# Performance work log

Hardware: AMD Instinct MI355X
Metric: run time of the kernel (lower is better)

Reference implementation:

```python
import jax, jax.numpy as jnp
import numpy as np

B, N, L = 1, 2048, 256
H, E = 24, 128
D = H * E          # query_dim = inner_dim = 3072
P = 1536           # added_kv_proj_dim
EPS = 1e-5


def _rope_tables(n, e):
    pos = np.arange(n, dtype=np.float32)
    inv_freq = 1.0 / (10000.0 ** (np.arange(0, e, 2, dtype=np.float32) / e))
    ang = pos[:, None] * inv_freq[None, :]          # [n, e/2]
    ang = np.repeat(ang, 2, axis=-1)                # interleaved pairs -> [n, e]
    return np.cos(ang).astype(np.float32), np.sin(ang).astype(np.float32)


def _trans_mat(e):
    # rotate-pairs matrix: (x @ tm)[2i] = -x[2i+1], (x @ tm)[2i+1] = x[2i]
    tm = np.zeros((e, e), dtype=np.float32)
    idx = np.arange(0, e, 2)
    tm[idx + 1, idx] = -1.0
    tm[idx, idx + 1] = 1.0
    return tm


def setup_inputs() -> dict:
    key = jax.random.key(0)
    ks = jax.random.split(key, 16)
    s = 0.02
    cos, sin = _rope_tables(N, E)
    return {
        "spatial": jax.random.normal(ks[0], (B, N, D), jnp.float32),
        "prompt": jax.random.normal(ks[1], (B, L, P), jnp.float32),
        "w_qkv": jax.random.normal(ks[2], (D, 3 * D), jnp.float32) * s,
        "w_add_qkv": jax.random.normal(ks[3], (P, 3 * D), jnp.float32) * s,
        "b_add_qkv": jax.random.normal(ks[4], (3 * D,), jnp.float32) * s,
        "norm_q_w": jnp.ones((E,), jnp.float32),
        "norm_k_w": jnp.ones((E,), jnp.float32),
        "norm_add_q_w": jnp.ones((E,), jnp.float32),
        "norm_add_k_w": jnp.ones((E,), jnp.float32),
        "w_out": jax.random.normal(ks[5], (D, D), jnp.float32) * s,
        "b_out": jax.random.normal(ks[6], (D,), jnp.float32) * s,
        "w_add_out": jax.random.normal(ks[7], (D, D), jnp.float32) * s,
        "b_add_out": jax.random.normal(ks[8], (D,), jnp.float32) * s,
        "rope_cos": jnp.asarray(cos),
        "rope_sin": jnp.asarray(sin),
        "trans_mat": jnp.asarray(_trans_mat(E)),
        "N": N,
    }


def _rms(x, w):
    return x * jax.lax.rsqrt(jnp.mean(x * x, axis=-1, keepdims=True) + EPS) * w


def _split_heads(x, h, e):
    b, s, _ = x.shape
    return x.reshape(b, s, h, e).transpose(0, 2, 1, 3)  # [B,H,S,E]


def reference(spatial, prompt, w_qkv, w_add_qkv, b_add_qkv,
              norm_q_w, norm_k_w, norm_add_q_w, norm_add_k_w,
              w_out, b_out, w_add_out, b_add_out,
              rope_cos, rope_sin, trans_mat, N):
    e = norm_q_w.shape[0]
    h = w_qkv.shape[1] // (3 * e)
    b, n, _ = spatial.shape

    # fused QKV for spatial stream (no bias)
    q, k, v = jnp.split(spatial @ w_qkv, 3, axis=-1)
    q, k, v = (_split_heads(t, h, e) for t in (q, k, v))   # [B,H,N,E]
    q = _rms(q, norm_q_w)
    k = _rms(k, norm_k_w)

    # fused QKV for prompt stream (with bias)
    aq, ak, av = jnp.split(prompt @ w_add_qkv + b_add_qkv, 3, axis=-1)
    aq, ak, av = (_split_heads(t, h, e) for t in (aq, ak, av))  # [B,H,L,E]
    aq = _rms(aq, norm_add_q_w)
    ak = _rms(ak, norm_add_k_w)

    # RoPE on spatial q/k: x*cos + (x@trans_mat)*sin
    def rope(x):
        return x * rope_cos + jnp.einsum('bhne,ef->bhnf', x, trans_mat) * rope_sin
    q = rope(q)
    k = rope(k)

    # joint attention, 'rear' strategy: prompt KV appended after spatial KV
    qf = jnp.concatenate([q, aq], axis=2)   # [B,H,N+L,E]
    kf = jnp.concatenate([k, ak], axis=2)
    vf = jnp.concatenate([v, av], axis=2)
    scale = 1.0 / jnp.sqrt(jnp.float32(e))
    scores = jnp.einsum('bhqe,bhke->bhqk', qf, kf) * scale
    attn = jax.nn.softmax(scores, axis=-1)
    out = jnp.einsum('bhqk,bhke->bhqe', attn, vf)           # [B,H,N+L,E]

    def merge(x):
        return x.transpose(0, 2, 1, 3).reshape(b, x.shape[2], h * e)

    spatial_out = merge(out[:, :, :n]) @ w_out + b_out      # [B,N,D]
    prompt_out = merge(out[:, :, n:]) @ w_add_out + b_add_out  # [B,L,D]
    return spatial_out, prompt_out
```

## Files before the change

### kernel.cpp

```cpp
#include <hip/hip_runtime.h>
#include <cstdint>
#include <cstddef>

typedef __attribute__((ext_vector_type(8))) short short8;
typedef __attribute__((ext_vector_type(4))) float f32x4;
typedef __attribute__((ext_vector_type(16))) float f32x16;

#define DEVI static __device__ __forceinline__

DEVI float bf2f(unsigned short b) {
  union { unsigned int u; float f; } v; v.u = ((unsigned int)b) << 16; return v.f;
}
DEVI unsigned short f2bf(float f) {
  union { float f; unsigned int u; } v; v.f = f;
  unsigned int r = v.u + 0x7fffu + ((v.u >> 16) & 1u);
  return (unsigned short)(r >> 16);
}
DEVI unsigned int pk2(float a, float b) {
  union { float f; unsigned int u; } ua, ub; ua.f = a; ub.f = b;
  return ((ua.u + 0x8000u) >> 16) | ((ub.u + 0x8000u) & 0xffff0000u);
}

DEVI void gload16(const void* g, void* l) {
  __builtin_amdgcn_global_load_lds(
      (const __attribute__((address_space(1))) void*)g,
      (__attribute__((address_space(3))) void*)l, 16, 0, 0);
}

DEVI void drain_ldsdma() {
  asm volatile("s_waitcnt vmcnt(0)" ::: "memory");
  __builtin_amdgcn_sched_barrier(0);
}

__global__ __launch_bounds__(256) void f32_to_bf16_2(
    const float* __restrict__ a, unsigned short* __restrict__ oa, int n4a,
    const float* __restrict__ b, unsigned short* __restrict__ ob, int n4b)
{
  int i = blockIdx.x * blockDim.x + threadIdx.x;
  int stride = gridDim.x * blockDim.x;
  int total = n4a + n4b;
  for (; i < total; i += stride) {
    const float4* src = (i < n4a) ? &((const float4*)a)[i] : &((const float4*)b)[i - n4a];
    ushort4* dst = (i < n4a) ? &((ushort4*)oa)[i] : &((ushort4*)ob)[i - n4a];
    float4 f = *src;
    ushort4 u;
    u.x = f2bf(f.x); u.y = f2bf(f.y); u.z = f2bf(f.z); u.w = f2bf(f.w);
    *dst = u;
  }
}

DEVI void tr_body(const float* in, unsigned short* out, int Kd, int Nd,
                  int n0, int k0, unsigned short (*tile)[72], int t)
{
  int r = t >> 2, cg = (t & 3) * 16;
  const float* src = in + (size_t)(k0 + r) * Nd + n0 + cg;
#pragma unroll
  for (int q = 0; q < 16; q += 4) {
    float4 f = *(const float4*)(src + q);
    ushort4 u;
    u.x = f2bf(f.x); u.y = f2bf(f.y); u.z = f2bf(f.z); u.w = f2bf(f.w);
    *(ushort4*)&tile[r][cg + q] = u;
  }
  __syncthreads();
  unsigned int p[8];
#pragma unroll
  for (int q = 0; q < 8; ++q)
    p[q] = (unsigned int)tile[cg + 2*q][r] | ((unsigned int)tile[cg + 2*q + 1][r] << 16);
  unsigned short* dst = out + (size_t)(n0 + r) * Kd + k0 + cg;
  *(uint4*)dst       = make_uint4(p[0], p[1], p[2], p[3]);
  *(uint4*)(dst + 8) = make_uint4(p[4], p[5], p[6], p[7]);
}

__global__ __launch_bounds__(256) void transpose_wqkv(
    const float* __restrict__ w_qkv, const float* __restrict__ w_add_qkv,
    unsigned short* __restrict__ wTq, unsigned short* __restrict__ wTaq)
{
  __shared__ unsigned short tile[64][72];
  int y = blockIdx.y;
  const float* in;  unsigned short* out;  int Kd, k0;
  if (y < 48) { in = w_qkv;     out = wTq;  Kd = 3072; k0 = y * 64; }
  else        { in = w_add_qkv; out = wTaq; Kd = 1536; k0 = (y - 48) * 64; }
  tr_body(in, out, Kd, 9216, blockIdx.x * 64, k0, tile, threadIdx.x);
}

__global__ __launch_bounds__(256) void transpose_wout(
    const float* __restrict__ w_out, const float* __restrict__ w_add_out,
    unsigned short* __restrict__ wTo, unsigned short* __restrict__ wTao)
{
  __shared__ unsigned short tile[64][72];
  const float* in = blockIdx.z ? w_add_out : w_out;
  unsigned short* out = blockIdx.z ? wTao : wTo;
  tr_body(in, out, 3072, 3072, blockIdx.x * 64, blockIdx.y * 64, tile, threadIdx.x);
}

__global__ __launch_bounds__(256) void transpose_bf16_64(
    const unsigned short* __restrict__ in, unsigned short* __restrict__ out,
    int rows, int cols)
{
  __shared__ unsigned short tile[64][72];
  size_t hoff = (size_t)blockIdx.z * rows * cols;
  int e0 = blockIdx.x * 64, s0 = blockIdx.y * 64;
  int t = threadIdx.x;
  int r = t >> 2, cg = (t & 3) * 16;
  const unsigned short* src = in + hoff + (size_t)(s0 + r) * cols + e0 + cg;
  *(uint4*)&tile[r][cg]     = *(const uint4*)src;
  *(uint4*)&tile[r][cg + 8] = *(const uint4*)(src + 8);
  __syncthreads();
  unsigned int p[8];
#pragma unroll
  for (int q = 0; q < 8; ++q)
    p[q] = (unsigned int)tile[cg + 2*q][r] | ((unsigned int)tile[cg + 2*q + 1][r] << 16);
  unsigned short* dst = out + hoff + (size_t)(e0 + r) * rows + s0 + cg;
  *(uint4*)dst       = make_uint4(p[0], p[1], p[2], p[3]);
  *(uint4*)(dst + 8) = make_uint4(p[4], p[5], p[6], p[7]);
}

__global__ __launch_bounds__(256, 4) void gemm_qkv2(
    const unsigned short* __restrict__ Aspat, const unsigned short* __restrict__ Aprom,
    const unsigned short* __restrict__ Btq, const unsigned short* __restrict__ Btaq,
    const float* __restrict__ biasp, unsigned short* __restrict__ Cout)
{
  __shared__ unsigned short lsA[128 * 64];
  __shared__ unsigned short lsB[128 * 64];
  const int tid = threadIdx.x;
  const int w = tid >> 6, lane = tid & 63;
  const int wr = w >> 1, wc = w & 1;
  const int l15 = lane & 15, lhi = lane >> 4;
  const int wg = blockIdx.x;
  const int swz = (wg & 7) * 162 + (wg >> 3);
  const int bx = swz / 18, by = swz - bx * 18;
  const bool pr = by >= 16;
  const int K = pr ? 1536 : 3072;

  f32x4 acc[4][4];
#pragma unroll
  for (int i = 0; i < 4; ++i)
#pragma unroll
    for (int j = 0; j < 4; ++j) acc[i][j] = (f32x4){0.f, 0.f, 0.f, 0.f};

  int srcoff[4];
#pragma unroll
  for (int j = 0; j < 4; ++j) {
    int c = j * 256 + tid;
    int row = c >> 3;
    int sl = (c & 7) ^ (row & 7);
    srcoff[j] = row * K + sl * 8;
  }
  const int wb = w * 1024;
  const unsigned short* Abase = pr ? (Aprom + (size_t)((by - 16) * 128) * 1536)
                                   : (Aspat + (size_t)(by * 128) * 3072);
  const unsigned short* Bbase = (pr ? Btaq : Btq) + (size_t)(bx * 128) * K;

  for (int k0 = 0; k0 < K; k0 += 64) {
#pragma unroll
    for (int j = 0; j < 4; ++j) {
      gload16(Abase + srcoff[j] + k0, (char*)lsA + j * 4096 + wb);
      gload16(Bbase + srcoff[j] + k0, (char*)lsB + j * 4096 + wb);
    }
    __syncthreads();
#pragma unroll
    for (int kk = 0; kk < 2; ++kk) {
      const int sl = ((kk << 2) + lhi) ^ (l15 & 7);
      short8 af[4], bf[4];
#pragma unroll
      for (int t = 0; t < 4; ++t) {
        af[t] = *(const short8*)((char*)lsA + (wr * 64 + t * 16 + l15) * 128 + (sl << 4));
        bf[t] = *(const short8*)((char*)lsB + (wc * 64 + t * 16 + l15) * 128 + (sl << 4));
      }
#pragma unroll
      for (int mt = 0; mt < 4; ++mt)
#pragma unroll
        for (int nt = 0; nt < 4; ++nt)
          acc[mt][nt] = __builtin_amdgcn_mfma_f32_16x16x32_bf16(af[mt], bf[nt], acc[mt][nt], 0, 0, 0);
    }
    __syncthreads();
  }

  const int nbase = bx * 128 + wc * 64;
  const int mbase = by * 128 + wr * 64;
  float bv[4] = {0.f, 0.f, 0.f, 0.f};
  if (pr) {
#pragma unroll
    for (int nt = 0; nt < 4; ++nt) bv[nt] = biasp[nbase + nt * 16 + l15];
  }
#pragma unroll
  for (int mt = 0; mt < 4; ++mt)
#pragma unroll
    for (int nt = 0; nt < 4; ++nt) {
#pragma unroll
      for (int r2 = 0; r2 < 4; ++r2) {
        int m = mbase + mt * 16 + lhi * 4 + r2;
        int n = nbase + nt * 16 + l15;
        Cout[(size_t)m * 9216 + n] = f2bf(acc[mt][nt][r2] + bv[nt]);
      }
    }
}

__global__ __launch_bounds__(256, 4) void gemm_out2(
    const unsigned short* __restrict__ A,
    const unsigned short* __restrict__ Bt0, const float* __restrict__ b0,
    const unsigned short* __restrict__ Bt1, const float* __restrict__ b1,
    float* __restrict__ C)
{
  __shared__ unsigned short lsA[128 * 64];
  __shared__ unsigned short lsB[128 * 64];
  const int tid = threadIdx.x;
  const int w = tid >> 6, lane = tid & 63;
  const int wr = w >> 1, wc = w & 1;
  const int l15 = lane & 15, lhi = lane >> 4;
  const int wg = blockIdx.x;
  const int swz = (wg & 7) * 54 + (wg >> 3);
  const int bx = swz / 18, by = swz - bx * 18;
  const bool pr = by >= 16;

  f32x4 acc[4][4];
#pragma unroll
  for (int i = 0; i < 4; ++i)
#pragma unroll
    for (int j = 0; j < 4; ++j) acc[i][j] = (f32x4){0.f, 0.f, 0.f, 0.f};

  int srcoff[4];
#pragma unroll
  for (int j = 0; j < 4; ++j) {
    int c = j * 256 + tid;
    int row = c >> 3;
    int sl = (c & 7) ^ (row & 7);
    srcoff[j] = row * 3072 + sl * 8;
  }
  const int wb = w * 1024;
  const unsigned short* Abase = A + (size_t)(by * 128) * 3072;
  const unsigned short* Bbase = (pr ? Bt1 : Bt0) + (size_t)(bx * 128) * 3072;
  const float* bias = pr ? b1 : b0;

  for (int k0 = 0; k0 < 3072; k0 += 64) {
#pragma unroll
    for (int j = 0; j < 4; ++j) {
      gload16(Abase + srcoff[j] + k0, (char*)lsA + j * 4096 + wb);
      gload16(Bbase + srcoff[j] + k0, (char*)lsB + j * 4096 + wb);
    }
    __syncthreads();
#pragma unroll
    for (int kk = 0; kk < 2; ++kk) {
      const int sl = ((kk << 2) + lhi) ^ (l15 & 7);
      short8 af[4], bf[4];
#pragma unroll
      for (int t = 0; t < 4; ++t) {
        af[t] = *(const short8*)((char*)lsA + (wr * 64 + t * 16 + l15) * 128 + (sl << 4));
        bf[t] = *(const short8*)((char*)lsB + (wc * 64 + t * 16 + l15) * 128 + (sl << 4));
      }
#pragma unroll
      for (int mt = 0; mt < 4; ++mt)
#pragma unroll
        for (int nt = 0; nt < 4; ++nt)
          acc[mt][nt] = __builtin_amdgcn_mfma_f32_16x16x32_bf16(af[mt], bf[nt], acc[mt][nt], 0, 0, 0);
    }
    __syncthreads();
  }

  const int nbase = bx * 128 + wc * 64;
  const int mbase = by * 128 + wr * 64;
  float bv[4];
#pragma unroll
  for (int nt = 0; nt < 4; ++nt) bv[nt] = bias[nbase + nt * 16 + l15];
#pragma unroll
  for (int mt = 0; mt < 4; ++mt)
#pragma unroll
    for (int nt = 0; nt < 4; ++nt) {
#pragma unroll
      for (int r2 = 0; r2 < 4; ++r2) {
        int m = mbase + mt * 16 + lhi * 4 + r2;
        int n = nbase + nt * 16 + l15;
        C[(size_t)m * 3072 + n] = acc[mt][nt][r2] + bv[nt];
      }
    }
}

__global__ __launch_bounds__(256) void fuse_rms_rope(
    const unsigned short* __restrict__ qkv,
    const unsigned short* __restrict__ aqkv,
    const float* __restrict__ nq, const float* __restrict__ nk,
    const float* __restrict__ naq, const float* __restrict__ nak,
    const float* __restrict__ ctab, const float* __restrict__ stab,
    unsigned short* __restrict__ Qf, unsigned short* __restrict__ Kf,
    unsigned short* __restrict__ Vf)
{
  int wid = blockIdx.x * 4 + (threadIdx.x >> 6);
  int lane = threadIdx.x & 63;
  int h = wid / 2304, s = wid % 2304;
  bool sp = (s < 2048);
  const unsigned short* src = sp ? (qkv + (size_t)s * 9216)
                                 : (aqkv + (size_t)(s - 2048) * 9216);
  int e = lane * 2;
  ushort2 qu = *(const ushort2*)&src[h * 128 + e];
  ushort2 ku = *(const ushort2*)&src[3072 + h * 128 + e];
  ushort2 vu = *(const ushort2*)&src[6144 + h * 128 + e];
  float q0 = bf2f(qu.x), q1 = bf2f(qu.y);
  float k0 = bf2f(ku.x), k1 = bf2f(ku.y);
  float sq = q0 * q0 + q1 * q1, sk = k0 * k0 + k1 * k1;
#pragma unroll
  for (int mm = 1; mm < 64; mm <<= 1) {
    sq += __shfl_xor(sq, mm);
    sk += __shfl_xor(sk, mm);
  }
  float rq = rsqrtf(sq * (1.f / 128.f) + 1e-5f);
  float rk = rsqrtf(sk * (1.f / 128.f) + 1e-5f);
  const float* wq = sp ? nq : naq;
  const float* wk = sp ? nk : nak;
  q0 *= rq * wq[e]; q1 *= rq * wq[e + 1];
  k0 *= rk * wk[e]; k1 *= rk * wk[e + 1];
  if (sp) {
    float c0 = ctab[s * 128 + e], c1 = ctab[s * 128 + e + 1];
    float s0 = stab[s * 128 + e], s1 = stab[s * 128 + e + 1];
    float a0 = q0 * c0 - q1 * s0, a1 = q1 * c1 + q0 * s1;
    float b0 = k0 * c0 - k1 * s0, b1 = k1 * c1 + k0 * s1;
    q0 = a0; q1 = a1; k0 = b0; k1 = b1;
  }
  const float scale = 0.08838834764831845f * 1.4426950408889634f;
  q0 *= scale; q1 *= scale;
  size_t o = (size_t)h * 2304 * 128 + (size_t)s * 128 + e;
  *(ushort2*)&Qf[o] = make_ushort2(f2bf(q0), f2bf(q1));
  *(ushort2*)&Kf[o] = make_ushort2(f2bf(k0), f2bf(k1));
  *(ushort2*)&Vf[o] = vu;
}

__global__ __launch_bounds__(256, 2) void attn_fwd(
    const unsigned short* __restrict__ Qf, const unsigned short* __restrict__ Kf,
    const unsigned short* __restrict__ Vt, unsigned short* __restrict__ Om)
{
  __shared__ unsigned short lsK[2][64 * 128];
  __shared__ unsigned short lsV[2][128 * 64];
  int wg = blockIdx.x;
  int swz = (wg & 7) * 54 + (wg >> 3);
  int h = swz / 18, qt = swz - h * 18;
  int q0 = qt * 128;
  int tid = threadIdx.x, w = tid >> 6, lane = tid & 63;
  int l31 = lane & 31, hh = lane >> 5;
  const size_t headO = (size_t)h * 2304 * 128;

  short8 qf[8];
  {
    const unsigned short* qrow = Qf + headO + (size_t)(q0 + w * 32 + l31) * 128 + hh * 8;
#pragma unroll
    for (int s = 0; s < 8; ++s)
      qf[s] = *(const short8*)(qrow + s * 16);
  }

  float m_run = -1e30f, lsum = 0.f;
  f32x16 accO[4];
#pragma unroll
  for (int dt = 0; dt < 4; ++dt)
#pragma unroll
    for (int i = 0; i < 16; ++i) accO[dt][i] = 0.f;

  size_t kGo[4], vGo[4];
  int loff[4];
#pragma unroll
  for (int j = 0; j < 4; ++j) {
    int c = j * 256 + w * 64 + lane;
    int krow = c >> 4, kcol = (c & 15) ^ (krow & 7);
    int vrow = c >> 3, vcol = (c & 7) ^ (vrow & 7);
    kGo[j] = (size_t)krow * 128 + kcol * 8;
    vGo[j] = (size_t)vrow * 2304 + vcol * 8;
    loff[j] = (j * 256 + w * 64) * 16;
  }
  const unsigned short* kbase0 = Kf + headO;
  const unsigned short* vbase0 = Vt + headO;

  auto stage = [&](int kb2, int b) {
    const unsigned short* kb_ = kbase0 + (size_t)kb2 * 128;
    const unsigned short* vb_ = vbase0 + kb2;
#pragma unroll
    for (int j = 0; j < 4; ++j) {
      gload16(kb_ + kGo[j], (char*)lsK[b] + loff[j]);
      gload16(vb_ + vGo[j], (char*)lsV[b] + loff[j]);
    }
  };

  stage(0, 0);
  int cur = 0;

  for (int kb = 0; kb < 2304; kb += 64) {
    drain_ldsdma();
    __syncthreads();
    if (kb + 64 < 2304) stage(kb + 64, cur ^ 1);

    f32x16 accS[2];
#pragma unroll
    for (int t = 0; t < 2; ++t)
#pragma unroll
      for (int i = 0; i < 16; ++i) accS[t][i] = 0.f;
    __builtin_amdgcn_s_setprio(1);
#pragma unroll
    for (int t = 0; t < 2; ++t) {
      const int row = l31 + t * 32;
      const int rsw = row & 7;
#pragma unroll
      for (int s = 0; s < 8; ++s) {
        short8 kfr = *(const short8*)((char*)lsK[cur] + row * 256 +
                        (((s * 2 + hh) ^ rsw) << 4));
        accS[t] = __builtin_amdgcn_mfma_f32_32x32x16_bf16(kfr, qf[s], accS[t], 0, 0, 0);
      }
    }
    __builtin_amdgcn_s_setprio(0);

    float lm = accS[0][0];
#pragma unroll
    for (int t = 0; t < 2; ++t)
#pragma unroll
      for (int i = 0; i < 16; ++i) lm = fmaxf(lm, accS[t][i]);
    float lmx = fmaxf(lm, __shfl_xor(lm, 32));
    if (!__all(lmx <= m_run + 11.0f)) {
      float mnew = fmaxf(m_run, lmx);
      float corr = __builtin_amdgcn_exp2f(m_run - mnew);
      lsum *= corr;
      float corrq[16];
#pragma unroll
      for (int r = 0; r < 16; ++r)
        corrq[r] = __shfl(corr, ((r & 3) + 8 * (r >> 2) + 4 * hh) | (lane & 32));
#pragma unroll
      for (int dt = 0; dt < 4; ++dt)
#pragma unroll
        for (int r = 0; r < 16; ++r) accO[dt][r] *= corrq[r];
      m_run = mnew;
    }
#pragma unroll
    for (int t = 0; t < 2; ++t)
#pragma unroll
      for (int i = 0; i < 16; ++i) {
        float p = __builtin_amdgcn_exp2f(accS[t][i] - m_run);
        accS[t][i] = p;
        lsum += p;
      }

    __builtin_amdgcn_s_setprio(1);
#pragma unroll
    for (int ks = 0; ks < 4; ++ks) {
      const int t = ks >> 1;
      const int qlo = 8 * (ks & 1);
      unsigned int wlo0 = pk2(accS[t][qlo + 0], accS[t][qlo + 1]);
      unsigned int wlo1 = pk2(accS[t][qlo + 2], accS[t][qlo + 3]);
      unsigned int whi0 = pk2(accS[t][qlo + 4], accS[t][qlo + 5]);
      unsigned int whi1 = pk2(accS[t][qlo + 6], accS[t][qlo + 7]);
      unsigned int r0 = __shfl_xor(hh ? wlo0 : whi0, 32);
      unsigned int r1 = __shfl_xor(hh ? wlo1 : whi1, 32);
      unsigned int fw0 = hh ? r0 : wlo0;
      unsigned int fw1 = hh ? r1 : wlo1;
      unsigned int fw2 = hh ? whi0 : r0;
      unsigned int fw3 = hh ? whi1 : r1;
      unsigned int fwa[4] = {fw0, fw1, fw2, fw3};
      short8 paf = *(short8*)fwa;
#pragma unroll
      for (int dt = 0; dt < 4; ++dt) {
        const int row = dt * 32 + l31;
        short8 vfr = *(const short8*)((char*)lsV[cur] + row * 128 +
                        (((ks * 2 + hh) ^ (row & 7)) << 4));
        accO[dt] = __builtin_amdgcn_mfma_f32_32x32x16_bf16(paf, vfr, accO[dt], 0, 0, 0);
      }
    }
    __builtin_amdgcn_s_setprio(0);
    cur ^= 1;
  }

  lsum += __shfl_xor(lsum, 32);
  float inv = 1.0f / lsum;
  float invq[16];
#pragma unroll
  for (int r = 0; r < 16; ++r)
    invq[r] = __shfl(inv, ((r & 3) + 8 * (r >> 2) + 4 * hh) | (lane & 32));
#pragma unroll
  for (int dt = 0; dt < 4; ++dt)
#pragma unroll
    for (int r = 0; r < 16; ++r) {
      int qrow = (r & 3) + 8 * (r >> 2) + 4 * hh;
      int row = q0 + w * 32 + qrow;
      Om[(size_t)row * 3072 + h * 128 + dt * 32 + l31] = f2bf(accO[dt][r] * invq[r]);
    }
}

extern "C" void kernel_launch(void* const* d_in, const int* in_sizes, int n_in,
                              void* d_out, int out_size, void* d_ws, size_t ws_size,
                              hipStream_t stream)
{
  const float* spatial      = (const float*)d_in[0];
  const float* prompt       = (const float*)d_in[1];
  const float* w_qkv        = (const float*)d_in[2];
  const float* w_add_qkv    = (const float*)d_in[3];
  const float* b_add_qkv    = (const float*)d_in[4];
  const float* norm_q_w     = (const float*)d_in[5];
  const float* norm_k_w     = (const float*)d_in[6];
  const float* norm_add_q_w = (const float*)d_in[7];
  const float* norm_add_k_w = (const float*)d_in[8];
  const float* w_out        = (const float*)d_in[9];
  const float* b_out        = (const float*)d_in[10];
  const float* w_add_out    = (const float*)d_in[11];
  const float* b_add_out    = (const float*)d_in[12];
  const float* rope_cos     = (const float*)d_in[13];
  const float* rope_sin     = (const float*)d_in[14];

  constexpr size_t O_WTQ  = 0;
  constexpr size_t O_WTAQ = 56623104;
  constexpr size_t O_SPAT = 84934656;
  constexpr size_t O_PROM = 97517568;
  constexpr size_t O_QKV  = 98304000;
  constexpr size_t O_AQKV = 136052736;
  constexpr size_t O_QF   = 140771328;
  constexpr size_t O_KF   = 154927104;
  constexpr size_t O_VF   = 169082880;
  constexpr size_t TOTAL  = 183238656;
  constexpr size_t O_WTO  = O_WTQ;
  constexpr size_t O_WTAO = O_WTQ + 18874368;
  constexpr size_t O_VT   = O_QKV;
  constexpr size_t O_ATTN = O_WTAQ;
  if (ws_size < TOTAL) return;

  char* ws = (char*)d_ws;
  unsigned short* wTq      = (unsigned short*)(ws + O_WTQ);
  unsigned short* wTaq     = (unsigned short*)(ws + O_WTAQ);
  unsigned short* spat_bf  = (unsigned short*)(ws + O_SPAT);
  unsigned short* prom_bf  = (unsigned short*)(ws + O_PROM);
  unsigned short* qkv_s    = (unsigned short*)(ws + O_QKV);
  unsigned short* aqkv     = (unsigned short*)(ws + O_AQKV);
  unsigned short* Qf       = (unsigned short*)(ws + O_QF);
  unsigned short* Kf       = (unsigned short*)(ws + O_KF);
  unsigned short* Vf       = (unsigned short*)(ws + O_VF);
  unsigned short* wTo      = (unsigned short*)(ws + O_WTO);
  unsigned short* wTao     = (unsigned short*)(ws + O_WTAO);
  unsigned short* Vt       = (unsigned short*)(ws + O_VT);
  unsigned short* attn_out = (unsigned short*)(ws + O_ATTN);

  f32_to_bf16_2<<<2048, 256, 0, stream>>>(spatial, spat_bf, 2048 * 3072 / 4,
                                          prompt, prom_bf, 256 * 1536 / 4);
  transpose_wqkv<<<dim3(144, 72), 256, 0, stream>>>(w_qkv, w_add_qkv, wTq, wTaq);
  gemm_qkv2<<<1296, 256, 0, stream>>>(spat_bf, prom_bf, wTq, wTaq, b_add_qkv, qkv_s);
  fuse_rms_rope<<<13824, 256, 0, stream>>>(qkv_s, aqkv, norm_q_w, norm_k_w,
                                           norm_add_q_w, norm_add_k_w,
                                           rope_cos, rope_sin, Qf, Kf, Vf);
  transpose_bf16_64<<<dim3(2, 36, 24), 256, 0, stream>>>(Vf, Vt, 2304, 128);
  attn_fwd<<<432, 256, 0, stream>>>(Qf, Kf, Vt, attn_out);
  transpose_wout<<<dim3(48, 48, 2), 256, 0, stream>>>(w_out, w_add_out, wTo, wTao);
  gemm_out2<<<432, 256, 0, stream>>>(attn_out, wTo, b_out, wTao, b_add_out,
                                     (float*)d_out);
}
```

Measured before the change: 401.4 us.

## Double query rows per wave in attention to reuse K/V LDS fragments

Each wave now handles two 32-row query blocks (256 query rows per workgroup) and keeps two sets of online-softmax state and output accumulators. Every K and V fragment read from LDS feeds two MFMAs, which halves LDS reads and K/V global staging per query. The grid shrinks from 432 to 216 workgroups and launch bounds drop to one block per SIMD. This raises register pressure and cuts occupancy and parallelism on a device with 256 CUs.

```diff
diff --git a/kernel.cpp b/kernel.cpp
--- a/kernel.cpp
+++ b/kernel.cpp
@@ -323,34 +323,37 @@
   *(ushort2*)&Vf[o] = vu;
 }
 
-__global__ __launch_bounds__(256, 2) void attn_fwd(
+__global__ __launch_bounds__(256, 1) void attn_fwd(
     const unsigned short* __restrict__ Qf, const unsigned short* __restrict__ Kf,
     const unsigned short* __restrict__ Vt, unsigned short* __restrict__ Om)
 {
   __shared__ unsigned short lsK[2][64 * 128];
   __shared__ unsigned short lsV[2][128 * 64];
   int wg = blockIdx.x;
-  int swz = (wg & 7) * 54 + (wg >> 3);
-  int h = swz / 18, qt = swz - h * 18;
-  int q0 = qt * 128;
+  int swz = (wg & 7) * 27 + (wg >> 3);
+  int h = swz / 9, qt = swz - h * 9;
+  int q0 = qt * 256;
   int tid = threadIdx.x, w = tid >> 6, lane = tid & 63;
   int l31 = lane & 31, hh = lane >> 5;
   const size_t headO = (size_t)h * 2304 * 128;
 
-  short8 qf[8];
+  short8 qfa[8], qfb[8];
   {
-    const unsigned short* qrow = Qf + headO + (size_t)(q0 + w * 32 + l31) * 128 + hh * 8;
-#pragma unroll
-    for (int s = 0; s < 8; ++s)
-      qf[s] = *(const short8*)(qrow + s * 16);
-  }
-
-  float m_run = -1e30f, lsum = 0.f;
-  f32x16 accO[4];
+    const unsigned short* qra = Qf + headO + (size_t)(q0 + w * 64 + l31) * 128 + hh * 8;
+    const unsigned short* qrb = qra + 32 * 128;
+#pragma unroll
+    for (int s = 0; s < 8; ++s) {
+      qfa[s] = *(const short8*)(qra + s * 16);
+      qfb[s] = *(const short8*)(qrb + s * 16);
+    }
+  }
+
+  float m0 = -1e30f, m1 = -1e30f, ls0 = 0.f, ls1 = 0.f;
+  f32x16 accO0[4], accO1[4];
 #pragma unroll
   for (int dt = 0; dt < 4; ++dt)
 #pragma unroll
-    for (int i = 0; i < 16; ++i) accO[dt][i] = 0.f;
+    for (int i = 0; i < 16; ++i) { accO0[dt][i] = 0.f; accO1[dt][i] = 0.f; }
 
   size_t kGo[4], vGo[4];
   int loff[4];
@@ -384,96 +387,144 @@
     __syncthreads();
     if (kb + 64 < 2304) stage(kb + 64, cur ^ 1);
 
-    f32x16 accS[2];
-#pragma unroll
-    for (int t = 0; t < 2; ++t)
-#pragma unroll
-      for (int i = 0; i < 16; ++i) accS[t][i] = 0.f;
-    __builtin_amdgcn_s_setprio(1);
 #pragma unroll
     for (int t = 0; t < 2; ++t) {
-      const int row = l31 + t * 32;
-      const int rsw = row & 7;
-#pragma unroll
-      for (int s = 0; s < 8; ++s) {
-        short8 kfr = *(const short8*)((char*)lsK[cur] + row * 256 +
-                        (((s * 2 + hh) ^ rsw) << 4));
-        accS[t] = __builtin_amdgcn_mfma_f32_32x32x16_bf16(kfr, qf[s], accS[t], 0, 0, 0);
-      }
-    }
-    __builtin_amdgcn_s_setprio(0);
-
-    float lm = accS[0][0];
-#pragma unroll
-    for (int t = 0; t < 2; ++t)
-#pragma unroll
-      for (int i = 0; i < 16; ++i) lm = fmaxf(lm, accS[t][i]);
-    float lmx = fmaxf(lm, __shfl_xor(lm, 32));
-    if (!__all(lmx <= m_run + 11.0f)) {
-      float mnew = fmaxf(m_run, lmx);
-      float corr = __builtin_amdgcn_exp2f(m_run - mnew);
-      lsum *= corr;
-      float corrq[16];
-#pragma unroll
-      for (int r = 0; r < 16; ++r)
-        corrq[r] = __shfl(corr, ((r & 3) + 8 * (r >> 2) + 4 * hh) | (lane & 32));
-#pragma unroll
-      for (int dt = 0; dt < 4; ++dt)
-#pragma unroll
-        for (int r = 0; r < 16; ++r) accO[dt][r] *= corrq[r];
-      m_run = mnew;
-    }
-#pragma unroll
-    for (int t = 0; t < 2; ++t)
-#pragma unroll
-      for (int i = 0; i < 16; ++i) {
-        float p = __builtin_amdgcn_exp2f(accS[t][i] - m_run);
-        accS[t][i] = p;
-        lsum += p;
-      }
-
-    __builtin_amdgcn_s_setprio(1);
-#pragma unroll
-    for (int ks = 0; ks < 4; ++ks) {
-      const int t = ks >> 1;
-      const int qlo = 8 * (ks & 1);
-      unsigned int wlo0 = pk2(accS[t][qlo + 0], accS[t][qlo + 1]);
-      unsigned int wlo1 = pk2(accS[t][qlo + 2], accS[t][qlo + 3]);
-      unsigned int whi0 = pk2(accS[t][qlo + 4], accS[t][qlo + 5]);
-      unsigned int whi1 = pk2(accS[t][qlo + 6], accS[t][qlo + 7]);
-      unsigned int r0 = __shfl_xor(hh ? wlo0 : whi0, 32);
-      unsigned int r1 = __shfl_xor(hh ? wlo1 : whi1, 32);
-      unsigned int fw0 = hh ? r0 : wlo0;
-      unsigned int fw1 = hh ? r1 : wlo1;
-      unsigned int fw2 = hh ? whi0 : r0;
-      unsigned int fw3 = hh ? whi1 : r1;
-      unsigned int fwa[4] = {fw0, fw1, fw2, fw3};
-      short8 paf = *(short8*)fwa;
-#pragma unroll
-      for (int dt = 0; dt < 4; ++dt) {
-        const int row = dt * 32 + l31;
-        short8 vfr = *(const short8*)((char*)lsV[cur] + row * 128 +
-                        (((ks * 2 + hh) ^ (row & 7)) << 4));
-        accO[dt] = __builtin_amdgcn_mfma_f32_32x32x16_bf16(paf, vfr, accO[dt], 0, 0, 0);
-      }
-    }
-    __builtin_amdgcn_s_setprio(0);
+      f32x16 aS0, aS1;
+#pragma unroll
+      for (int i = 0; i < 16; ++i) { aS0[i] = 0.f; aS1[i] = 0.f; }
+
+      __builtin_amdgcn_s_setprio(1);
+      {
+        const int row = l31 + t * 32;
+        const int rsw = row & 7;
+#pragma unroll
+        for (int s = 0; s < 8; ++s) {
+          short8 kfr = *(const short8*)((char*)lsK[cur] + row * 256 +
+                          (((s * 2 + hh) ^ rsw) << 4));
+          aS0 = __builtin_amdgcn_mfma_f32_32x32x16_bf16(kfr, qfa[s], aS0, 0, 0, 0);
+          aS1 = __builtin_amdgcn_mfma_f32_32x32x16_bf16(kfr, qfb[s], aS1, 0, 0, 0);
+        }
+      }
+      __builtin_amdgcn_s_setprio(0);
+
+      {
+        float lm = aS0[0];
+#pragma unroll
+        for (int i = 1; i < 16; ++i) lm = fmaxf(lm, aS0[i]);
+        float lmx = fmaxf(lm, __shfl_xor(lm, 32));
+        if (!__all(lmx <= m0 + 11.0f)) {
+          float mnew = fmaxf(m0, lmx);
+          float corr = __builtin_amdgcn_exp2f(m0 - mnew);
+          ls0 *= corr;
+          float corrq[16];
+#pragma unroll
+          for (int r = 0; r < 16; ++r)
+            corrq[r] = __shfl(corr, ((r & 3) + 8 * (r >> 2) + 4 * hh) | (lane & 32));
+#pragma unroll
+          for (int dt = 0; dt < 4; ++dt)
+#pragma unroll
+            for (int r = 0; r < 16; ++r) accO0[dt][r] *= corrq[r];
+          m0 = mnew;
+        }
+#pragma unroll
+        for (int i = 0; i < 16; ++i) {
+          float p = __builtin_amdgcn_exp2f(aS0[i] - m0);
+          aS0[i] = p;
+          ls0 += p;
+        }
+      }
+      {
+        float lm = aS1[0];
+#pragma unroll
+        for (int i = 1; i < 16; ++i) lm = fmaxf(lm, aS1[i]);
+        float lmx = fmaxf(lm, __shfl_xor(lm, 32));
+        if (!__all(lmx <= m1 + 11.0f)) {
+          float mnew = fmaxf(m1, lmx);
+          float corr = __builtin_amdgcn_exp2f(m1 - mnew);
+          ls1 *= corr;
+          float corrq[16];
+#pragma unroll
+          for (int r = 0; r < 16; ++r)
+            corrq[r] = __shfl(corr, ((r & 3) + 8 * (r >> 2) + 4 * hh) | (lane & 32));
+#pragma unroll
+          for (int dt = 0; dt < 4; ++dt)
+#pragma unroll
+            for (int r = 0; r < 16; ++r) accO1[dt][r] *= corrq[r];
+          m1 = mnew;
+        }
+#pragma unroll
+        for (int i = 0; i < 16; ++i) {
+          float p = __builtin_amdgcn_exp2f(aS1[i] - m1);
+          aS1[i] = p;
+          ls1 += p;
+        }
+      }
+
+      __builtin_amdgcn_s_setprio(1);
+#pragma unroll
+      for (int ks2 = 0; ks2 < 2; ++ks2) {
+        const int qlo = 8 * ks2;
+        unsigned int a_lo0 = pk2(aS0[qlo + 0], aS0[qlo + 1]);
+        unsigned int a_lo1 = pk2(aS0[qlo + 2], aS0[qlo + 3]);
+        unsigned int a_hi0 = pk2(aS0[qlo + 4], aS0[qlo + 5]);
+        unsigned int a_hi1 = pk2(aS0[qlo + 6], aS0[qlo + 7]);
+        unsigned int ar0 = __shfl_xor(hh ? a_lo0 : a_hi0, 32);
+        unsigned int ar1 = __shfl_xor(hh ? a_lo1 : a_hi1, 32);
+        unsigned int afw[4];
+        afw[0] = hh ? ar0 : a_lo0;
+        afw[1] = hh ? ar1 : a_lo1;
+        afw[2] = hh ? a_hi0 : ar0;
+        afw[3] = hh ? a_hi1 : ar1;
+        short8 paf0 = *(short8*)afw;
+
+        unsigned int b_lo0 = pk2(aS1[qlo + 0], aS1[qlo + 1]);
+        unsigned int b_lo1 = pk2(aS1[qlo + 2], aS1[qlo + 3]);
+        unsigned int b_hi0 = pk2(aS1[qlo + 4], aS1[qlo + 5]);
+        unsigned int b_hi1 = pk2(aS1[qlo + 6], aS1[qlo + 7]);
+        unsigned int br0 = __shfl_xor(hh ? b_lo0 : b_hi0, 32);
+        unsigned int br1 = __shfl_xor(hh ? b_lo1 : b_hi1, 32);
+        unsigned int bfw[4];
+        bfw[0] = hh ? br0 : b_lo0;
+        bfw[1] = hh ? br1 : b_lo1;
+        bfw[2] = hh ? b_hi0 : br0;
+        bfw[3] = hh ? b_hi1 : br1;
+        short8 paf1 = *(short8*)bfw;
+
+        const int ksg = t * 2 + ks2;
+#pragma unroll
+        for (int dt = 0; dt < 4; ++dt) {
+          const int row = dt * 32 + l31;
+          short8 vfr = *(const short8*)((char*)lsV[cur] + row * 128 +
+                          (((ksg * 2 + hh) ^ (row & 7)) << 4));
+          accO0[dt] = __builtin_amdgcn_mfma_f32_32x32x16_bf16(paf0, vfr, accO0[dt], 0, 0, 0);
+          accO1[dt] = __builtin_amdgcn_mfma_f32_32x32x16_bf16(paf1, vfr, accO1[dt], 0, 0, 0);
+        }
+      }
+      __builtin_amdgcn_s_setprio(0);
+    }
     cur ^= 1;
   }
 
-  lsum += __shfl_xor(lsum, 32);
-  float inv = 1.0f / lsum;
-  float invq[16];
-#pragma unroll
-  for (int r = 0; r < 16; ++r)
-    invq[r] = __shfl(inv, ((r & 3) + 8 * (r >> 2) + 4 * hh) | (lane & 32));
+  ls0 += __shfl_xor(ls0, 32);
+  ls1 += __shfl_xor(ls1, 32);
+  float inv0 = 1.0f / ls0;
+  float inv1 = 1.0f / ls1;
+  float invq0[16], invq1[16];
+#pragma unroll
+  for (int r = 0; r < 16; ++r) {
+    int srcl = ((r & 3) + 8 * (r >> 2) + 4 * hh) | (lane & 32);
+    invq0[r] = __shfl(inv0, srcl);
+    invq1[r] = __shfl(inv1, srcl);
+  }
 #pragma unroll
   for (int dt = 0; dt < 4; ++dt)
 #pragma unroll
     for (int r = 0; r < 16; ++r) {
       int qrow = (r & 3) + 8 * (r >> 2) + 4 * hh;
-      int row = q0 + w * 32 + qrow;
-      Om[(size_t)row * 3072 + h * 128 + dt * 32 + l31] = f2bf(accO[dt][r] * invq[r]);
+      int rowa = q0 + w * 64 + qrow;
+      int rowb = rowa + 32;
+      Om[(size_t)rowa * 3072 + h * 128 + dt * 32 + l31] = f2bf(accO0[dt][r] * invq0[r]);
+      Om[(size_t)rowb * 3072 + h * 128 + dt * 32 + l31] = f2bf(accO1[dt][r] * invq1[r]);
     }
 }
 
@@ -536,7 +587,7 @@
                                            norm_add_q_w, norm_add_k_w,
                                            rope_cos, rope_sin, Qf, Kf, Vf);
   transpose_bf16_64<<<dim3(2, 36, 24), 256, 0, stream>>>(Vf, Vt, 2304, 128);
-  attn_fwd<<<432, 256, 0, stream>>>(Qf, Kf, Vt, attn_out);
+  attn_fwd<<<216, 256, 0, stream>>>(Qf, Kf, Vt, attn_out);
   transpose_wout<<<dim3(48, 48, 2), 256, 0, stream>>>(w_out, w_add_out, wTo, wTao);
   gemm_out2<<<432, 256, 0, stream>>>(attn_out, wTo, b_out, wTao, b_add_out,
                                      (float*)d_out);
```

New measurement: 440.1 us. 1.1x slower.
